# Optimization experiments

Hardware: AMD Instinct MI355X
Metric: run time of the kernel (lower is better)

The kernel has to match this reference:

```python
import jax, jax.numpy as jnp
import numpy as np

H = 1024

def setup_inputs() -> dict:
    key = jax.random.key(0)
    ks = jax.random.split(key, 7)
    s = 1.0 / np.sqrt(H)
    return {
        "hidden_states": jax.random.normal(ks[0], (4, 2048, H), dtype=jnp.float32),
        "Wq": jax.random.uniform(ks[1], (H, H), jnp.float32, -s, s),
        "bq": jax.random.uniform(ks[2], (H,), jnp.float32, -s, s),
        "Wk": jax.random.uniform(ks[3], (H, H), jnp.float32, -s, s),
        "bk": jax.random.uniform(ks[4], (H,), jnp.float32, -s, s),
        "Wv": jax.random.uniform(ks[5], (H, H), jnp.float32, -s, s),
        "bv": jax.random.uniform(ks[6], (H,), jnp.float32, -s, s),
    }

def reference(hidden_states, Wq, bq, Wk, bk, Wv, bv):
    # Linear projections (torch Linear: x @ W.T + b)
    q = hidden_states @ Wq.T + bq  # [B,S,H]
    k = hidden_states @ Wk.T + bk
    v = hidden_states @ Wv.T + bv
    # Unscaled attention
    probs = jax.nn.softmax(jnp.einsum("bqh,bkh->bqk", q, k), axis=-1)  # [B,S,S]
    attention_scores = jnp.sum(probs, axis=-2)  # [B,S] column sums
    context = jnp.einsum("bqk,bkh->bqh", probs, v)  # [B,S,H]
    return (context, attention_scores)
```

## Files before the change

### kernel.cpp

```cpp
#include <hip/hip_runtime.h>
#include <stdint.h>


typedef __attribute__((ext_vector_type(8))) short short8;
typedef __attribute__((ext_vector_type(4))) float floatx4;
typedef __attribute__((ext_vector_type(4))) unsigned short ushort4v;
typedef unsigned short u16;

__device__ __forceinline__ u16 f2bf(float f) {
  union { float f; uint32_t u; } v; v.f = f;
  uint32_t u = v.u;
  return (u16)((u + 0x7FFFu + ((u >> 16) & 1u)) >> 16);
}
__device__ __forceinline__ float bf2f(u16 h) {
  union { uint32_t u; float f; } v; v.u = ((uint32_t)h) << 16; return v.f;
}

#define AS3(p) ((__attribute__((address_space(3))) void*)(uint32_t)(uintptr_t)(p))
#define AS1(p) ((__attribute__((address_space(1))) void*)(uintptr_t)(p))

__global__ __launch_bounds__(256) void cvt_kernel(const float* __restrict__ src,
                                                  u16* __restrict__ dst, int n) {
  int i = (blockIdx.x * 256 + threadIdx.x) * 4;
  if (i < n) {
    const float4 v = *(const float4*)(src + i);
    ushort4v o;
    o[0] = f2bf(v.x); o[1] = f2bf(v.y); o[2] = f2bf(v.z); o[3] = f2bf(v.w);
    *(ushort4v*)(dst + i) = o;
  }
}

__global__ __launch_bounds__(256) void cvtW_kernel(const float* __restrict__ Wq,
                                                   const float* __restrict__ Wk,
                                                   const float* __restrict__ Wv,
                                                   u16* __restrict__ dst) {
  const float* src = (blockIdx.y == 0) ? Wq : (blockIdx.y == 1) ? Wk : Wv;
  int i = (blockIdx.x * 256 + threadIdx.x) * 4;
  const float4 v = *(const float4*)(src + i);
  ushort4v o;
  o[0] = f2bf(v.x); o[1] = f2bf(v.y); o[2] = f2bf(v.z); o[3] = f2bf(v.w);
  *(ushort4v*)(dst + blockIdx.y * 1048576 + i) = o;
}

__device__ __forceinline__ void gemm_core(const u16* __restrict__ A,
                                          const u16* __restrict__ B,
                                          int lda, int ldb, int K,
                                          u16* As, u16* Bs, floatx4 acc[4][4]) {
  const int tid  = threadIdx.x;
  const int lane = tid & 63;
  const int w    = tid >> 6;
  const int wr   = (w >> 1) * 64;
  const int wc   = (w & 1) * 64;
  const int fr   = lane & 15;
  const int quad = lane >> 4;

  const u16* pa[4];
  const u16* pb[4];
#pragma unroll
  for (int j = 0; j < 4; ++j) {
    const int q   = tid + j * 256;
    const int row = q >> 3, col = q & 7;
    const int gc  = col ^ (row & 7);
    pa[j] = A + row * lda + gc * 8;
    pb[j] = B + row * ldb + gc * 8;
  }

  for (int kk = 0; kk < K; kk += 64) {
#pragma unroll
    for (int j = 0; j < 4; ++j) {
      __builtin_amdgcn_global_load_lds(AS1(pa[j]), AS3(As + (tid + j * 256) * 8), 16, 0, 0);
      __builtin_amdgcn_global_load_lds(AS1(pb[j]), AS3(Bs + (tid + j * 256) * 8), 16, 0, 0);
      pa[j] += 64; pb[j] += 64;
    }
    __syncthreads();
#pragma unroll
    for (int ks = 0; ks < 2; ++ks) {
      const int pc = ((ks * 4 + quad) ^ (fr & 7)) * 8;
      short8 af[4], bfr[4];
#pragma unroll
      for (int i = 0; i < 4; ++i) {
        af[i]  = *(const short8*)(As + (wr + i * 16 + fr) * 64 + pc);
        bfr[i] = *(const short8*)(Bs + (wc + i * 16 + fr) * 64 + pc);
      }
#pragma unroll
      for (int mi = 0; mi < 4; ++mi)
#pragma unroll
        for (int ni = 0; ni < 4; ++ni)
          acc[mi][ni] = __builtin_amdgcn_mfma_f32_16x16x32_bf16(af[mi], bfr[ni],
                                                                acc[mi][ni], 0, 0, 0);
    }
    __syncthreads();
  }
}

__global__ __launch_bounds__(256) void proj_kernel(
    const u16* __restrict__ hsb, const u16* __restrict__ Wb,
    const float* __restrict__ bq, const float* __restrict__ bk,
    const float* __restrict__ bv,
    u16* __restrict__ qo, u16* __restrict__ ko, u16* __restrict__ vt) {
  __shared__ __align__(16) u16 As[8192];
  __shared__ __align__(16) u16 Bs[8192];
  floatx4 acc[4][4];
#pragma unroll
  for (int i = 0; i < 4; ++i)
#pragma unroll
    for (int j = 0; j < 4; ++j) acc[i][j] = {0.f, 0.f, 0.f, 0.f};

  const int p  = blockIdx.z;
  const int m0 = blockIdx.x * 128;
  const int n0 = blockIdx.y * 128;
  gemm_core(hsb + m0 * 1024, Wb + p * 1048576 + n0 * 1024, 1024, 1024, 1024, As, Bs, acc);

  const float* bias = (p == 0) ? bq : (p == 1) ? bk : bv;
  const int lane = threadIdx.x & 63, w = threadIdx.x >> 6;
  const int wr = (w >> 1) * 64, wc = (w & 1) * 64;
  const int col = lane & 15, rg4 = (lane >> 4) * 4;

  if (p < 2) {
    u16* out = (p == 0) ? qo : ko;
#pragma unroll
    for (int mi = 0; mi < 4; ++mi)
#pragma unroll
      for (int ni = 0; ni < 4; ++ni) {
        const int n = n0 + wc + ni * 16 + col;
        const float bn = bias[n];
#pragma unroll
        for (int r = 0; r < 4; ++r) {
          const int m = m0 + wr + mi * 16 + rg4 + r;
          out[m * 1024 + n] = f2bf(acc[mi][ni][r] + bn);
        }
      }
  } else {
#pragma unroll
    for (int mi = 0; mi < 4; ++mi) {
      const int mbase = m0 + wr + mi * 16 + rg4;
      const int b = mbase >> 11, s = mbase & 2047;
#pragma unroll
      for (int ni = 0; ni < 4; ++ni) {
        const int n = n0 + wc + ni * 16 + col;
        const float bn = bias[n];
        ushort4v pk;
#pragma unroll
        for (int r = 0; r < 4; ++r) pk[r] = f2bf(acc[mi][ni][r] + bn);
        *(ushort4v*)(vt + b * 2097152 + n * 2048 + s) = pk;
      }
    }
  }
}

__global__ __launch_bounds__(256) void logits_kernel(
    const u16* __restrict__ q, const u16* __restrict__ k,
    u16* __restrict__ E, float* __restrict__ lsum) {
  __shared__ __align__(16) u16 As[8192];
  __shared__ __align__(16) u16 Bs[8192];
  floatx4 acc[4][4];
#pragma unroll
  for (int i = 0; i < 4; ++i)
#pragma unroll
    for (int j = 0; j < 4; ++j) acc[i][j] = {0.f, 0.f, 0.f, 0.f};

  const int b  = blockIdx.z;
  const int m0 = blockIdx.y * 128;
  const int n0 = blockIdx.x * 128;
  gemm_core(q + (b * 2048 + m0) * 1024, k + (b * 2048 + n0) * 1024,
            1024, 1024, 1024, As, Bs, acc);

  const int lane = threadIdx.x & 63, w = threadIdx.x >> 6;
  const int wr = (w >> 1) * 64, wc = (w & 1) * 64;
  const int col = lane & 15, rg4 = (lane >> 4) * 4;
  u16* Eb = E + b * 4194304;
  float* lb = lsum + b * 2048;

#pragma unroll
  for (int mi = 0; mi < 4; ++mi) {
    floatx4 rs = {0.f, 0.f, 0.f, 0.f};
    const int rbase = m0 + wr + mi * 16 + rg4;
#pragma unroll
    for (int ni = 0; ni < 4; ++ni) {
      const int n = n0 + wc + ni * 16 + col;
#pragma unroll
      for (int r = 0; r < 4; ++r) {
        const float e = __expf(acc[mi][ni][r]);
        rs[r] += e;
        Eb[(rbase + r) * 2048 + n] = f2bf(e);
      }
    }
#pragma unroll
    for (int off = 1; off < 16; off <<= 1) {
      rs[0] += __shfl_xor(rs[0], off, 64);
      rs[1] += __shfl_xor(rs[1], off, 64);
      rs[2] += __shfl_xor(rs[2], off, 64);
      rs[3] += __shfl_xor(rs[3], off, 64);
    }
    if ((lane & 15) == 0) {
#pragma unroll
      for (int r = 0; r < 4; ++r) atomicAdd(&lb[rbase + r], rs[r]);
    }
  }
}

__global__ __launch_bounds__(256) void context_kernel(
    const u16* __restrict__ E, const u16* __restrict__ vt,
    const float* __restrict__ lsum, float* __restrict__ out) {
  __shared__ __align__(16) u16 As[8192];
  __shared__ __align__(16) u16 Bs[8192];
  floatx4 acc[4][4];
#pragma unroll
  for (int i = 0; i < 4; ++i)
#pragma unroll
    for (int j = 0; j < 4; ++j) acc[i][j] = {0.f, 0.f, 0.f, 0.f};

  const int b  = blockIdx.z;
  const int m0 = blockIdx.y * 128;
  const int n0 = blockIdx.x * 128;
  gemm_core(E + b * 4194304 + m0 * 2048, vt + b * 2097152 + n0 * 2048,
            2048, 2048, 2048, As, Bs, acc);

  const int lane = threadIdx.x & 63, w = threadIdx.x >> 6;
  const int wr = (w >> 1) * 64, wc = (w & 1) * 64;
  const int col = lane & 15, rg4 = (lane >> 4) * 4;
  const float* lb = lsum + b * 2048;

#pragma unroll
  for (int mi = 0; mi < 4; ++mi) {
    const int rbase = m0 + wr + mi * 16 + rg4;
    float rinv[4];
#pragma unroll
    for (int r = 0; r < 4; ++r) rinv[r] = 1.0f / lb[rbase + r];
#pragma unroll
    for (int ni = 0; ni < 4; ++ni) {
      const int n = n0 + wc + ni * 16 + col;
#pragma unroll
      for (int r = 0; r < 4; ++r)
        out[(b * 2048 + rbase + r) * 1024 + n] = acc[mi][ni][r] * rinv[r];
    }
  }
}

__global__ __launch_bounds__(256) void colsum_kernel(
    const u16* __restrict__ E, const float* __restrict__ lsum,
    float* __restrict__ scores) {
  const int b  = blockIdx.x;
  const int q0 = blockIdx.y * 32;
  const int j  = threadIdx.x * 8;
  const u16* Eb = E + b * 4194304;
  const float* lb = lsum + b * 2048;
  float acc[8];
#pragma unroll
  for (int c = 0; c < 8; ++c) acc[c] = 0.f;
  for (int r = 0; r < 32; ++r) {
    const int qi = q0 + r;
    const float rinv = 1.0f / lb[qi];
    const short8 ev = *(const short8*)(Eb + qi * 2048 + j);
#pragma unroll
    for (int c = 0; c < 8; ++c) acc[c] += bf2f((u16)ev[c]) * rinv;
  }
  float* sb = scores + b * 2048 + j;
#pragma unroll
  for (int c = 0; c < 8; ++c) atomicAdd(&sb[c], acc[c]);
}

extern "C" void kernel_launch(void* const* d_in, const int* in_sizes, int n_in,
                              void* d_out, int out_size, void* d_ws, size_t ws_size,
                              hipStream_t stream) {
  const float* hs = (const float*)d_in[0];
  const float* Wq = (const float*)d_in[1];
  const float* bq = (const float*)d_in[2];
  const float* Wk = (const float*)d_in[3];
  const float* bk = (const float*)d_in[4];
  const float* Wv = (const float*)d_in[5];
  const float* bv = (const float*)d_in[6];

  char* ws = (char*)d_ws;
  u16*   qw  = (u16*)(ws);
  u16*   kw  = (u16*)(ws + (16u << 20));
  u16*   vtw = (u16*)(ws + (32u << 20));
  float* lw  = (float*)(ws + (48u << 20));
  u16*   hsb = (u16*)(ws + (49u << 20));
  u16*   Wb  = (u16*)(ws + (65u << 20));
  u16*   Ew  = (u16*)(ws + (49u << 20));

  float* outc = (float*)d_out;
  float* outs = outc + 8388608;

  hipMemsetAsync(lw, 0, 8192 * sizeof(float), stream);
  hipMemsetAsync(outs, 0, 8192 * sizeof(float), stream);

  cvt_kernel<<<8192, 256, 0, stream>>>(hs, hsb, 8388608);
  cvtW_kernel<<<dim3(1024, 3), 256, 0, stream>>>(Wq, Wk, Wv, Wb);

  proj_kernel<<<dim3(64, 8, 3), 256, 0, stream>>>(hsb, Wb, bq, bk, bv, qw, kw, vtw);
  logits_kernel<<<dim3(16, 16, 4), 256, 0, stream>>>(qw, kw, Ew, lw);
  context_kernel<<<dim3(8, 16, 4), 256, 0, stream>>>(Ew, vtw, lw, outc);
  colsum_kernel<<<dim3(4, 64), 256, 0, stream>>>(Ew, lw, outs);
}
```

Baseline: 273.7 us.

## Switch GEMMs to 32x32x16 MFMA with 256x128 block tiles

Replaces the 16x16x32 MFMA core with 32x32x16 MFMA instructions and enlarges each block tile from 128x128 to 256x128, so each wave computes 128x64. Per MFMA, fewer LDS fragment loads are needed, and larger tiles reuse B data across more rows. The cost is twice the A-side LDS, more accumulator registers (128 floats per thread), and half as many blocks per grid. For the context kernel that means only 256 blocks, which may underfill the GPU. It also sets launch bounds to two blocks per CU.

```diff
diff --git a/kernel.cpp b/kernel.cpp
--- a/kernel.cpp
+++ b/kernel.cpp
@@ -4,6 +4,7 @@
 
 typedef __attribute__((ext_vector_type(8))) short short8;
 typedef __attribute__((ext_vector_type(4))) float floatx4;
+typedef __attribute__((ext_vector_type(16))) float floatx16;
 typedef __attribute__((ext_vector_type(4))) unsigned short ushort4v;
 typedef unsigned short u16;
 
@@ -45,196 +46,207 @@
 __device__ __forceinline__ void gemm_core(const u16* __restrict__ A,
                                           const u16* __restrict__ B,
                                           int lda, int ldb, int K,
-                                          u16* As, u16* Bs, floatx4 acc[4][4]) {
+                                          u16* As, u16* Bs, floatx16 acc[4][2]) {
   const int tid  = threadIdx.x;
   const int lane = tid & 63;
   const int w    = tid >> 6;
-  const int wr   = (w >> 1) * 64;
-  const int wc   = (w & 1) * 64;
-  const int fr   = lane & 15;
-  const int quad = lane >> 4;
-
-  const u16* pa[4];
-  const u16* pb[4];
-#pragma unroll
-  for (int j = 0; j < 4; ++j) {
-    const int q   = tid + j * 256;
-    const int row = q >> 3, col = q & 7;
-    const int gc  = col ^ (row & 7);
-    pa[j] = A + row * lda + gc * 8;
-    pb[j] = B + row * ldb + gc * 8;
-  }
+  const int wm   = (w >> 1) * 128;
+  const int wn   = (w & 1) * 64;
+  const int fr   = lane & 31;
+  const int half = lane >> 5;
+
+  const int row0 = tid >> 3;
+  const int gc   = (tid & 7) ^ (row0 & 7);
+  const u16* pa = A + row0 * lda + gc * 8;
+  const u16* pb = B + row0 * ldb + gc * 8;
 
   for (int kk = 0; kk < K; kk += 64) {
 #pragma unroll
-    for (int j = 0; j < 4; ++j) {
-      __builtin_amdgcn_global_load_lds(AS1(pa[j]), AS3(As + (tid + j * 256) * 8), 16, 0, 0);
-      __builtin_amdgcn_global_load_lds(AS1(pb[j]), AS3(Bs + (tid + j * 256) * 8), 16, 0, 0);
-      pa[j] += 64; pb[j] += 64;
-    }
+    for (int j = 0; j < 8; ++j)
+      __builtin_amdgcn_global_load_lds(AS1(pa + j * 32 * lda),
+                                       AS3(As + (tid + j * 256) * 8), 16, 0, 0);
+#pragma unroll
+    for (int j = 0; j < 4; ++j)
+      __builtin_amdgcn_global_load_lds(AS1(pb + j * 32 * ldb),
+                                       AS3(Bs + (tid + j * 256) * 8), 16, 0, 0);
+    pa += 64; pb += 64;
     __syncthreads();
 #pragma unroll
-    for (int ks = 0; ks < 2; ++ks) {
-      const int pc = ((ks * 4 + quad) ^ (fr & 7)) * 8;
-      short8 af[4], bfr[4];
-#pragma unroll
-      for (int i = 0; i < 4; ++i) {
-        af[i]  = *(const short8*)(As + (wr + i * 16 + fr) * 64 + pc);
-        bfr[i] = *(const short8*)(Bs + (wc + i * 16 + fr) * 64 + pc);
-      }
+    for (int ks = 0; ks < 4; ++ks) {
+      const int pc = ((ks * 2 + half) ^ (fr & 7)) * 8;
+      short8 af[4], bfr[2];
 #pragma unroll
       for (int mi = 0; mi < 4; ++mi)
-#pragma unroll
-        for (int ni = 0; ni < 4; ++ni)
-          acc[mi][ni] = __builtin_amdgcn_mfma_f32_16x16x32_bf16(af[mi], bfr[ni],
+        af[mi] = *(const short8*)(As + (wm + mi * 32 + fr) * 64 + pc);
+#pragma unroll
+      for (int ni = 0; ni < 2; ++ni)
+        bfr[ni] = *(const short8*)(Bs + (wn + ni * 32 + fr) * 64 + pc);
+#pragma unroll
+      for (int mi = 0; mi < 4; ++mi)
+#pragma unroll
+        for (int ni = 0; ni < 2; ++ni)
+          acc[mi][ni] = __builtin_amdgcn_mfma_f32_32x32x16_bf16(af[mi], bfr[ni],
                                                                 acc[mi][ni], 0, 0, 0);
     }
     __syncthreads();
   }
 }
 
-__global__ __launch_bounds__(256) void proj_kernel(
+__device__ __forceinline__ void acc_zero(floatx16 acc[4][2]) {
+#pragma unroll
+  for (int mi = 0; mi < 4; ++mi)
+#pragma unroll
+    for (int ni = 0; ni < 2; ++ni)
+#pragma unroll
+      for (int e = 0; e < 16; ++e) acc[mi][ni][e] = 0.f;
+}
+
+
+__global__ __launch_bounds__(256, 2) void proj_kernel(
     const u16* __restrict__ hsb, const u16* __restrict__ Wb,
     const float* __restrict__ bq, const float* __restrict__ bk,
     const float* __restrict__ bv,
     u16* __restrict__ qo, u16* __restrict__ ko, u16* __restrict__ vt) {
-  __shared__ __align__(16) u16 As[8192];
+  __shared__ __align__(16) u16 As[16384];
   __shared__ __align__(16) u16 Bs[8192];
-  floatx4 acc[4][4];
-#pragma unroll
-  for (int i = 0; i < 4; ++i)
-#pragma unroll
-    for (int j = 0; j < 4; ++j) acc[i][j] = {0.f, 0.f, 0.f, 0.f};
+  floatx16 acc[4][2];
+  acc_zero(acc);
 
   const int p  = blockIdx.z;
-  const int m0 = blockIdx.x * 128;
+  const int m0 = blockIdx.x * 256;
   const int n0 = blockIdx.y * 128;
   gemm_core(hsb + m0 * 1024, Wb + p * 1048576 + n0 * 1024, 1024, 1024, 1024, As, Bs, acc);
 
   const float* bias = (p == 0) ? bq : (p == 1) ? bk : bv;
   const int lane = threadIdx.x & 63, w = threadIdx.x >> 6;
-  const int wr = (w >> 1) * 64, wc = (w & 1) * 64;
-  const int col = lane & 15, rg4 = (lane >> 4) * 4;
+  const int wm = (w >> 1) * 128, wn = (w & 1) * 64;
+  const int fr = lane & 31, half = lane >> 5;
 
   if (p < 2) {
     u16* out = (p == 0) ? qo : ko;
 #pragma unroll
-    for (int mi = 0; mi < 4; ++mi)
-#pragma unroll
-      for (int ni = 0; ni < 4; ++ni) {
-        const int n = n0 + wc + ni * 16 + col;
-        const float bn = bias[n];
-#pragma unroll
-        for (int r = 0; r < 4; ++r) {
-          const int m = m0 + wr + mi * 16 + rg4 + r;
-          out[m * 1024 + n] = f2bf(acc[mi][ni][r] + bn);
+    for (int ni = 0; ni < 2; ++ni) {
+      const int n = n0 + wn + ni * 32 + fr;
+      const float bn = bias[n];
+#pragma unroll
+      for (int mi = 0; mi < 4; ++mi)
+#pragma unroll
+        for (int g = 0; g < 4; ++g) {
+          const int rowb = m0 + wm + mi * 32 + 8 * g + 4 * half;
+#pragma unroll
+          for (int r = 0; r < 4; ++r)
+            out[(rowb + r) * 1024 + n] = f2bf(acc[mi][ni][g * 4 + r] + bn);
         }
-      }
+    }
   } else {
 #pragma unroll
-    for (int mi = 0; mi < 4; ++mi) {
-      const int mbase = m0 + wr + mi * 16 + rg4;
-      const int b = mbase >> 11, s = mbase & 2047;
-#pragma unroll
-      for (int ni = 0; ni < 4; ++ni) {
-        const int n = n0 + wc + ni * 16 + col;
-        const float bn = bias[n];
-        ushort4v pk;
-#pragma unroll
-        for (int r = 0; r < 4; ++r) pk[r] = f2bf(acc[mi][ni][r] + bn);
-        *(ushort4v*)(vt + b * 2097152 + n * 2048 + s) = pk;
-      }
-    }
-  }
-}
-
-__global__ __launch_bounds__(256) void logits_kernel(
+    for (int ni = 0; ni < 2; ++ni) {
+      const int n = n0 + wn + ni * 32 + fr;
+      const float bn = bias[n];
+#pragma unroll
+      for (int mi = 0; mi < 4; ++mi)
+#pragma unroll
+        for (int g = 0; g < 4; ++g) {
+          const int m = m0 + wm + mi * 32 + 8 * g + 4 * half;
+          const int b = m >> 11, s = m & 2047;
+          ushort4v pk;
+#pragma unroll
+          for (int r = 0; r < 4; ++r) pk[r] = f2bf(acc[mi][ni][g * 4 + r] + bn);
+          *(ushort4v*)(vt + b * 2097152 + n * 2048 + s) = pk;
+        }
+    }
+  }
+}
+
+__global__ __launch_bounds__(256, 2) void logits_kernel(
     const u16* __restrict__ q, const u16* __restrict__ k,
     u16* __restrict__ E, float* __restrict__ lsum) {
-  __shared__ __align__(16) u16 As[8192];
+  __shared__ __align__(16) u16 As[16384];
   __shared__ __align__(16) u16 Bs[8192];
-  floatx4 acc[4][4];
-#pragma unroll
-  for (int i = 0; i < 4; ++i)
-#pragma unroll
-    for (int j = 0; j < 4; ++j) acc[i][j] = {0.f, 0.f, 0.f, 0.f};
+  floatx16 acc[4][2];
+  acc_zero(acc);
 
   const int b  = blockIdx.z;
-  const int m0 = blockIdx.y * 128;
+  const int m0 = blockIdx.y * 256;
   const int n0 = blockIdx.x * 128;
   gemm_core(q + (b * 2048 + m0) * 1024, k + (b * 2048 + n0) * 1024,
             1024, 1024, 1024, As, Bs, acc);
 
   const int lane = threadIdx.x & 63, w = threadIdx.x >> 6;
-  const int wr = (w >> 1) * 64, wc = (w & 1) * 64;
-  const int col = lane & 15, rg4 = (lane >> 4) * 4;
+  const int wm = (w >> 1) * 128, wn = (w & 1) * 64;
+  const int fr = lane & 31, half = lane >> 5;
   u16* Eb = E + b * 4194304;
   float* lb = lsum + b * 2048;
 
 #pragma unroll
   for (int mi = 0; mi < 4; ++mi) {
-    floatx4 rs = {0.f, 0.f, 0.f, 0.f};
-    const int rbase = m0 + wr + mi * 16 + rg4;
-#pragma unroll
-    for (int ni = 0; ni < 4; ++ni) {
-      const int n = n0 + wc + ni * 16 + col;
-#pragma unroll
-      for (int r = 0; r < 4; ++r) {
-        const float e = __expf(acc[mi][ni][r]);
-        rs[r] += e;
-        Eb[(rbase + r) * 2048 + n] = f2bf(e);
+    float rs[16];
+#pragma unroll
+    for (int e = 0; e < 16; ++e) rs[e] = 0.f;
+#pragma unroll
+    for (int ni = 0; ni < 2; ++ni) {
+      const int n = n0 + wn + ni * 32 + fr;
+#pragma unroll
+      for (int g = 0; g < 4; ++g) {
+        const int rowb = m0 + wm + mi * 32 + 8 * g + 4 * half;
+#pragma unroll
+        for (int r = 0; r < 4; ++r) {
+          const float e = __expf(acc[mi][ni][g * 4 + r]);
+          rs[g * 4 + r] += e;
+          Eb[(rowb + r) * 2048 + n] = f2bf(e);
+        }
       }
     }
 #pragma unroll
-    for (int off = 1; off < 16; off <<= 1) {
-      rs[0] += __shfl_xor(rs[0], off, 64);
-      rs[1] += __shfl_xor(rs[1], off, 64);
-      rs[2] += __shfl_xor(rs[2], off, 64);
-      rs[3] += __shfl_xor(rs[3], off, 64);
-    }
-    if ((lane & 15) == 0) {
-#pragma unroll
-      for (int r = 0; r < 4; ++r) atomicAdd(&lb[rbase + r], rs[r]);
-    }
-  }
-}
-
-__global__ __launch_bounds__(256) void context_kernel(
+    for (int off = 1; off < 32; off <<= 1)
+#pragma unroll
+      for (int e = 0; e < 16; ++e) rs[e] += __shfl_xor(rs[e], off, 64);
+    if (fr == 0) {
+#pragma unroll
+      for (int g = 0; g < 4; ++g) {
+        const int rowb = m0 + wm + mi * 32 + 8 * g + 4 * half;
+#pragma unroll
+        for (int r = 0; r < 4; ++r) atomicAdd(&lb[rowb + r], rs[g * 4 + r]);
+      }
+    }
+  }
+}
+
+__global__ __launch_bounds__(256, 2) void context_kernel(
     const u16* __restrict__ E, const u16* __restrict__ vt,
     const float* __restrict__ lsum, float* __restrict__ out) {
-  __shared__ __align__(16) u16 As[8192];
+  __shared__ __align__(16) u16 As[16384];
   __shared__ __align__(16) u16 Bs[8192];
-  floatx4 acc[4][4];
-#pragma unroll
-  for (int i = 0; i < 4; ++i)
-#pragma unroll
-    for (int j = 0; j < 4; ++j) acc[i][j] = {0.f, 0.f, 0.f, 0.f};
+  floatx16 acc[4][2];
+  acc_zero(acc);
 
   const int b  = blockIdx.z;
-  const int m0 = blockIdx.y * 128;
+  const int m0 = blockIdx.y * 256;
   const int n0 = blockIdx.x * 128;
   gemm_core(E + b * 4194304 + m0 * 2048, vt + b * 2097152 + n0 * 2048,
             2048, 2048, 2048, As, Bs, acc);
 
   const int lane = threadIdx.x & 63, w = threadIdx.x >> 6;
-  const int wr = (w >> 1) * 64, wc = (w & 1) * 64;
-  const int col = lane & 15, rg4 = (lane >> 4) * 4;
+  const int wm = (w >> 1) * 128, wn = (w & 1) * 64;
+  const int fr = lane & 31, half = lane >> 5;
   const float* lb = lsum + b * 2048;
 
 #pragma unroll
-  for (int mi = 0; mi < 4; ++mi) {
-    const int rbase = m0 + wr + mi * 16 + rg4;
-    float rinv[4];
-#pragma unroll
-    for (int r = 0; r < 4; ++r) rinv[r] = 1.0f / lb[rbase + r];
-#pragma unroll
-    for (int ni = 0; ni < 4; ++ni) {
-      const int n = n0 + wc + ni * 16 + col;
-#pragma unroll
-      for (int r = 0; r < 4; ++r)
-        out[(b * 2048 + rbase + r) * 1024 + n] = acc[mi][ni][r] * rinv[r];
-    }
-  }
+  for (int mi = 0; mi < 4; ++mi)
+#pragma unroll
+    for (int g = 0; g < 4; ++g) {
+      const int rowb = m0 + wm + mi * 32 + 8 * g + 4 * half;
+      float rinv[4];
+#pragma unroll
+      for (int r = 0; r < 4; ++r) rinv[r] = 1.0f / lb[rowb + r];
+#pragma unroll
+      for (int ni = 0; ni < 2; ++ni) {
+        const int n = n0 + wn + ni * 32 + fr;
+#pragma unroll
+        for (int r = 0; r < 4; ++r)
+          out[(b * 2048 + rowb + r) * 1024 + n] = acc[mi][ni][g * 4 + r] * rinv[r];
+      }
+    }
 }
 
 __global__ __launch_bounds__(256) void colsum_kernel(
@@ -289,8 +301,8 @@
   cvt_kernel<<<8192, 256, 0, stream>>>(hs, hsb, 8388608);
   cvtW_kernel<<<dim3(1024, 3), 256, 0, stream>>>(Wq, Wk, Wv, Wb);
 
-  proj_kernel<<<dim3(64, 8, 3), 256, 0, stream>>>(hsb, Wb, bq, bk, bv, qw, kw, vtw);
-  logits_kernel<<<dim3(16, 16, 4), 256, 0, stream>>>(qw, kw, Ew, lw);
-  context_kernel<<<dim3(8, 16, 4), 256, 0, stream>>>(Ew, vtw, lw, outc);
+  proj_kernel<<<dim3(32, 8, 3), 256, 0, stream>>>(hsb, Wb, bq, bk, bv, qw, kw, vtw);
+  logits_kernel<<<dim3(16, 8, 4), 256, 0, stream>>>(qw, kw, Ew, lw);
+  context_kernel<<<dim3(8, 8, 4), 256, 0, stream>>>(Ew, vtw, lw, outc);
   colsum_kernel<<<dim3(4, 64), 256, 0, stream>>>(Ew, lw, outs);
 }
```

New measurement: 305.9 us. +11.7%, slower.
